# Optimization experiments

Measured on AMD Instinct MI355X. Metric: run time of the kernel, lower is better.

The kernel has to match this reference:

```python
import jax, jax.numpy as jnp
import numpy as np
from jax import lax

KS = 3
N = KS * KS


def _conv(x, W, b, pad, stride):
    out = lax.conv_general_dilated(
        x, W, window_strides=(stride, stride),
        padding=[(pad, pad), (pad, pad)],
        dimension_numbers=("NCHW", "OIHW", "NCHW"))
    return out + b[None, :, None, None]


def setup_inputs() -> dict:
    key = jax.random.key(0)
    ks = jax.random.split(key, 5)
    b, c, h, w, outc = 16, 64, 64, 64, 128
    return {
        "x": jax.random.normal(ks[0], (b, c, h, w), jnp.float32),
        "W_off": jax.random.normal(ks[1], (2 * N, c, KS, KS), jnp.float32) * 0.05,
        "b_off": jax.random.normal(ks[2], (2 * N,), jnp.float32) * 0.05,
        "W_k": jax.random.normal(ks[3], (outc, c, KS, KS), jnp.float32) * 0.05,
        "b_k": jax.random.normal(ks[4], (outc,), jnp.float32) * 0.05,
    }


def _deform_conv(x, W_off, b_off, W_k, b_k):
    b, c, h, w = x.shape
    offset = _conv(x, W_off, b_off, pad=1, stride=1)  # [b, 2N, h, w]

    # kernel-grid offsets, flattened with x (row) index first: n = i*ks + j
    rng = jnp.arange(KS, dtype=x.dtype) - (KS - 1) // 2  # [-1, 0, 1]
    pnx = jnp.repeat(rng, KS)  # [N]
    pny = jnp.tile(rng, KS)    # [N]

    # sampling positions p = p0 + p_n + offset, clamped into the image
    px = jnp.arange(h, dtype=x.dtype)[None, None, :, None] + pnx[None, :, None, None] + offset[:, :N]
    py = jnp.arange(w, dtype=x.dtype)[None, None, None, :] + pny[None, :, None, None] + offset[:, N:]
    px = jnp.clip(px, 0, h - 1)
    py = jnp.clip(py, 0, w - 1)

    fx = jnp.floor(px)
    fy = jnp.floor(py)
    tx = px - fx  # fractional parts (bilinear weights)
    ty = py - fy
    x0 = fx.astype(jnp.int32)
    y0 = fy.astype(jnp.int32)
    x1 = jnp.minimum(x0 + 1, h - 1)  # out-of-range tap carries zero weight
    y1 = jnp.minimum(y0 + 1, w - 1)

    x_hw = x.transpose(0, 2, 3, 1).reshape(b, h * w, c)  # [b, hw, c]

    def gather(ix, iy):
        idx = (ix * w + iy).reshape(b, -1, 1)  # [b, N*h*w, 1]
        return jnp.take_along_axis(x_hw, idx, axis=1).reshape(b, N, h, w, c)

    wx0, wx1 = (1 - tx)[..., None], tx[..., None]
    wy0, wy1 = (1 - ty)[..., None], ty[..., None]
    # 4-tap bilinear interpolation == the original's sparse G @ x
    xo = (gather(x0, y0) * wx0 * wy0 + gather(x1, y0) * wx1 * wy0
          + gather(x0, y1) * wx0 * wy1 + gather(x1, y1) * wx1 * wy1)  # [b,N,h,w,c]

    # _reshape_x_offset: out[b,c, i_h*ks+i, i_w*ks+j] = xo[b, i*ks+j, i_h, i_w, c]
    xo = xo.reshape(b, KS, KS, h, w, c).transpose(0, 5, 3, 1, 4, 2)
    xo = xo.reshape(b, c, h * KS, w * KS)

    return _conv(xo, W_k, b_k, pad=0, stride=KS)  # [b, outc, h, w]


def reference(x, W_off, b_off, W_k, b_k):
    return _deform_conv(x, W_off, b_off, W_k, b_k)
```

## Files before the change

### kernel.cpp

```cpp
#include <hip/hip_runtime.h>

typedef __attribute__((ext_vector_type(8))) short bf16x8;
typedef __attribute__((ext_vector_type(4))) float floatx4;

__device__ __forceinline__ unsigned short f2bf(float f) {
    unsigned int u = __float_as_uint(f);
    u += 0x7FFFu + ((u >> 16) & 1u);
    return (unsigned short)(u >> 16);
}

__device__ __forceinline__ int interp_word(int a00, int a01, int a10, int a11,
                                           float w00, float w01, float w10, float w11) {
    float vl = w00 * __uint_as_float((unsigned)a00 << 16)
             + w01 * __uint_as_float((unsigned)a01 << 16)
             + w10 * __uint_as_float((unsigned)a10 << 16)
             + w11 * __uint_as_float((unsigned)a11 << 16);
    float vh = w00 * __uint_as_float((unsigned)a00 & 0xffff0000u)
             + w01 * __uint_as_float((unsigned)a01 & 0xffff0000u)
             + w10 * __uint_as_float((unsigned)a10 & 0xffff0000u)
             + w11 * __uint_as_float((unsigned)a11 & 0xffff0000u);
    return (int)__builtin_amdgcn_perm(__float_as_uint(vh) + 0x8000u,
                                      __float_as_uint(vl) + 0x8000u, 0x07060302u);
}

__global__ __launch_bounds__(256) void prep_all(const float* __restrict__ x,
        const float* __restrict__ Wk, const float* __restrict__ Woff,
        unsigned short* __restrict__ xt, unsigned short* __restrict__ Wkb2,
        unsigned short* __restrict__ Woffb) {
    int bb = blockIdx.x;
    if (bb < 1024) {
        __shared__ float tile[64][65];
        int b = bb >> 6, y = bb & 63;
        const float* src = x + (size_t)b * 262144 + y * 64;
        int tx = threadIdx.x & 15, tg = threadIdx.x >> 4;
#pragma unroll
        for (int i = 0; i < 4; i++) {
            int c = tg + i * 16;
            float4 v = *(const float4*)(src + (size_t)c * 4096 + tx * 4);
            tile[c][tx * 4 + 0] = v.x; tile[c][tx * 4 + 1] = v.y;
            tile[c][tx * 4 + 2] = v.z; tile[c][tx * 4 + 3] = v.w;
        }
        __syncthreads();
        unsigned short* dst = xt + (size_t)bb * 4096;
#pragma unroll
        for (int i = 0; i < 4; i++) {
            int xc = tg + i * 16;
            int c4 = tx * 4;
            ushort4 v;
            v.x = f2bf(tile[c4 + 0][xc]); v.y = f2bf(tile[c4 + 1][xc]);
            v.z = f2bf(tile[c4 + 2][xc]); v.w = f2bf(tile[c4 + 3][xc]);
            *(ushort4*)(dst + xc * 64 + c4) = v;
        }
    } else if (bb < 1312) {
        int idx = (bb - 1024) * 256 + threadIdx.x;
        int tap = idx >> 13;
        int r = idx & 8191;
        int tile = r >> 9;
        int ln = (r >> 3) & 63;
        int j = r & 7;
        int mt = tile >> 1, kc = tile & 1;
        int oc = mt * 16 + (ln & 15);
        int c = kc * 32 + (ln >> 4) * 8 + j;
        Wkb2[idx] = f2bf(Wk[(oc * 64 + c) * 9 + tap]);
    } else {
        int idx = (bb - 1312) * 256 + threadIdx.x;
        int tap = idx >> 11;
        int r = idx & 2047;
        int tile = r >> 9;
        int ln = (r >> 3) & 63;
        int j = r & 7;
        int mt = tile >> 1, kc = tile & 1;
        int n = mt * 16 + (ln & 15);
        int c = kc * 32 + (ln >> 4) * 8 + j;
        float v = (n < 18) ? Woff[(n * 64 + c) * 9 + tap] : 0.f;
        Woffb[idx] = f2bf(v);
    }
}

__global__ __launch_bounds__(256, 2) void fused_kernel(
        const unsigned short* __restrict__ xt,
        const unsigned short* __restrict__ Wkb2,
        const unsigned short* __restrict__ Woffb,
        const float* __restrict__ boff,
        const float* __restrict__ bias,
        float* __restrict__ out) {
    __shared__ float offs[64][20];
    int tid = threadIdx.x;
    int wave = tid >> 6, lane = tid & 63;
    int frow = lane & 15, quad = lane >> 4;
    int bb = blockIdx.x;
    int xcd = bb & 7, idx = bb >> 3;
    int b = xcd * 2 + (idx >> 6);
    int pxBase = (idx & 63) * 64;
    int pl = wave * 16 + frow;
    int px = pxBase + pl;
    int y = px >> 6, xx = px & 63;
    const char* img = (const char*)(xt + (size_t)b * 262144) + quad * 16;

    float bv[2][4];
#pragma unroll
    for (int mt = 0; mt < 2; mt++)
#pragma unroll
        for (int rg = 0; rg < 4; rg++) {
            int n = mt * 16 + quad * 4 + rg;
            bv[mt][rg] = (n < 18) ? boff[n] : 0.f;
        }

    floatx4 acc1[2];
    acc1[0] = (floatx4)(0.f); acc1[1] = (floatx4)(0.f);
#pragma unroll
    for (int tap = 0; tap < 9; tap++) {
        int ry = y + tap / 3 - 1, rx = xx + tap % 3 - 1;
        bool valid = (ry >= 0) & (ry < 64) & (rx >= 0) & (rx < 64);
        const char* src = img + ((ry * 64 + rx) << 7);
        const unsigned short* wofft = Woffb + tap * 2048 + lane * 8;
        bf16x8 bz = {};
#pragma unroll
        for (int kc = 0; kc < 2; kc++) {
            bf16x8 bfr = valid ? *(const bf16x8*)(src + kc * 64) : bz;
#pragma unroll
            for (int mt = 0; mt < 2; mt++) {
                bf16x8 af = *(const bf16x8*)(wofft + (mt * 2 + kc) * 512);
                acc1[mt] = __builtin_amdgcn_mfma_f32_16x16x32_bf16(af, bfr, acc1[mt], 0, 0, 0);
            }
        }
    }
#pragma unroll
    for (int mt = 0; mt < 2; mt++)
#pragma unroll
        for (int rg = 0; rg < 4; rg++) {
            int n = mt * 16 + quad * 4 + rg;
            if (n < 18) offs[pl][n] = acc1[mt][rg] + bv[mt][rg];
        }
    __syncthreads();

    floatx4 acc[8];
#pragma unroll
    for (int i = 0; i < 8; i++) acc[i] = (floatx4)(0.f);

    const float* op = &offs[pl][0];

    auto stage = [&](int tap, int4 (&r00)[2], int4 (&r01)[2], int4 (&r10)[2],
                     int4 (&r11)[2], floatx4& w) {
        float orow = op[tap];
        float ocol = op[9 + tap];
        float pr = (float)(y + tap / 3 - 1) + orow;
        float pc = (float)(xx + tap % 3 - 1) + ocol;
        pr = fminf(fmaxf(pr, 0.f), 63.f);
        pc = fminf(fmaxf(pc, 0.f), 63.f);
        float fr = floorf(pr), fc = floorf(pc);
        float tr = pr - fr, tc = pc - fc;
        int r0 = (int)fr, c0 = (int)fc;
        int r1 = min(r0 + 1, 63), c1 = min(c0 + 1, 63);
        w[0] = (1.f - tr) * (1.f - tc);
        w[1] = (1.f - tr) * tc;
        w[2] = tr * (1.f - tc);
        w[3] = tr * tc;
        const char* p00 = img + ((r0 * 64 + c0) << 7);
        const char* p01 = img + ((r0 * 64 + c1) << 7);
        const char* p10 = img + ((r1 * 64 + c0) << 7);
        const char* p11 = img + ((r1 * 64 + c1) << 7);
#pragma unroll
        for (int kc = 0; kc < 2; kc++) {
            r00[kc] = *(const int4*)(p00 + kc * 64);
            r01[kc] = *(const int4*)(p01 + kc * 64);
            r10[kc] = *(const int4*)(p10 + kc * 64);
            r11[kc] = *(const int4*)(p11 + kc * 64);
        }
    };

    int4 c00[2], c01[2], c10[2], c11[2];
    floatx4 cw;
    stage(0, c00, c01, c10, c11, cw);

#pragma unroll 1
    for (int tap = 0; tap < 9; tap++) {
        const unsigned short* wkt = Wkb2 + tap * 8192 + lane * 8;

        bf16x8 af0[8];
#pragma unroll
        for (int mt = 0; mt < 8; mt++)
            af0[mt] = *(const bf16x8*)(wkt + (mt * 2) * 512);

        int4 n00[2], n01[2], n10[2], n11[2];
        floatx4 nw;
        if (tap < 8)
            stage(tap + 1, n00, n01, n10, n11, nw);

        bf16x8 bfrag[2];
#pragma unroll
        for (int kc = 0; kc < 2; kc++) {
            int4 r;
            r.x = interp_word(c00[kc].x, c01[kc].x, c10[kc].x, c11[kc].x,
                              cw[0], cw[1], cw[2], cw[3]);
            r.y = interp_word(c00[kc].y, c01[kc].y, c10[kc].y, c11[kc].y,
                              cw[0], cw[1], cw[2], cw[3]);
            r.z = interp_word(c00[kc].z, c01[kc].z, c10[kc].z, c11[kc].z,
                              cw[0], cw[1], cw[2], cw[3]);
            r.w = interp_word(c00[kc].w, c01[kc].w, c10[kc].w, c11[kc].w,
                              cw[0], cw[1], cw[2], cw[3]);
            bfrag[kc] = __builtin_bit_cast(bf16x8, r);
        }

#pragma unroll
        for (int mt = 0; mt < 8; mt++)
            acc[mt] = __builtin_amdgcn_mfma_f32_16x16x32_bf16(af0[mt], bfrag[0], acc[mt], 0, 0, 0);

        bf16x8 af1[8];
#pragma unroll
        for (int mt = 0; mt < 8; mt++)
            af1[mt] = *(const bf16x8*)(wkt + (mt * 2 + 1) * 512);
#pragma unroll
        for (int mt = 0; mt < 8; mt++)
            acc[mt] = __builtin_amdgcn_mfma_f32_16x16x32_bf16(af1[mt], bfrag[1], acc[mt], 0, 0, 0);

        if (tap < 8) {
#pragma unroll
            for (int kc = 0; kc < 2; kc++) {
                c00[kc] = n00[kc]; c01[kc] = n01[kc];
                c10[kc] = n10[kc]; c11[kc] = n11[kc];
            }
            cw = nw;
        }
    }

    float* outb = out + (size_t)b * 524288 + px;
#pragma unroll
    for (int mt = 0; mt < 8; mt++) {
        float4 bc = *(const float4*)(bias + mt * 16 + quad * 4);
        float bcv[4] = {bc.x, bc.y, bc.z, bc.w};
#pragma unroll
        for (int rg = 0; rg < 4; rg++) {
            int oc = mt * 16 + quad * 4 + rg;
            outb[oc * 4096] = acc[mt][rg] + bcv[rg];
        }
    }
}

extern "C" void kernel_launch(void* const* d_in, const int* in_sizes, int n_in,
                              void* d_out, int out_size, void* d_ws, size_t ws_size,
                              hipStream_t stream) {
    const float* x    = (const float*)d_in[0];
    const float* Woff = (const float*)d_in[1];
    const float* boff = (const float*)d_in[2];
    const float* Wk   = (const float*)d_in[3];
    const float* bk   = (const float*)d_in[4];
    float* out = (float*)d_out;

    char* ws = (char*)d_ws;
    unsigned short* xt    = (unsigned short*)ws;
    unsigned short* Wkb2  = (unsigned short*)(ws + 8388608);
    unsigned short* Woffb = (unsigned short*)(ws + 8536064);

    prep_all<<<1384, 256, 0, stream>>>(x, Wk, Woff, xt, Wkb2, Woffb);
    fused_kernel<<<1024, 256, 0, stream>>>(xt, Wkb2, Woffb, boff, bk, out);
}
```

Measured before the change: 144.5 us.

## Double-buffer tap weights in LDS via async global-to-LDS loads

Per-tap Wk fragments are now staged into two LDS buffers with global_load_lds and read back from LDS for the MFMAs, replacing the per-lane global loads. The weight loads for the next tap overlap with the gather and interpolation for the current tap. Synchronisation uses a manual s_waitcnt vmcnt plus s_barrier, and occupancy is raised to 3 blocks per CU. Risks are about 32KB of extra LDS per block limiting occupancy, the hand-counted vmcnt being fragile, and the removed __syncthreads before offs is read relying on the first barrier inside the loop.

```diff
diff --git a/kernel.cpp b/kernel.cpp
--- a/kernel.cpp
+++ b/kernel.cpp
@@ -21,6 +21,12 @@
              + w11 * __uint_as_float((unsigned)a11 & 0xffff0000u);
     return (int)__builtin_amdgcn_perm(__float_as_uint(vh) + 0x8000u,
                                       __float_as_uint(vl) + 0x8000u, 0x07060302u);
+}
+
+__device__ __forceinline__ void g2l16(const unsigned short* g, unsigned short* l) {
+    __builtin_amdgcn_global_load_lds(
+        (const __attribute__((address_space(1))) unsigned int*)g,
+        (__attribute__((address_space(3))) unsigned int*)l, 16, 0, 0);
 }
 
 __global__ __launch_bounds__(256) void prep_all(const float* __restrict__ x,
@@ -77,13 +83,15 @@
     }
 }
 
-__global__ __launch_bounds__(256, 2) void fused_kernel(
+__global__ __launch_bounds__(256, 3) void fused_kernel(
         const unsigned short* __restrict__ xt,
         const unsigned short* __restrict__ Wkb2,
         const unsigned short* __restrict__ Woffb,
         const float* __restrict__ boff,
         const float* __restrict__ bias,
         float* __restrict__ out) {
+    __shared__ unsigned short As0[8192];
+    __shared__ unsigned short As1[8192];
     __shared__ float offs[64][20];
     int tid = threadIdx.x;
     int wave = tid >> 6, lane = tid & 63;
@@ -132,7 +140,6 @@
             int n = mt * 16 + quad * 4 + rg;
             if (n < 18) offs[pl][n] = acc1[mt][rg] + bv[mt][rg];
         }
-    __syncthreads();
 
     floatx4 acc[8];
 #pragma unroll
@@ -169,60 +176,75 @@
         }
     };
 
-    int4 c00[2], c01[2], c10[2], c11[2];
-    floatx4 cw;
-    stage(0, c00, c01, c10, c11, cw);
-
-#pragma unroll 1
-    for (int tap = 0; tap < 9; tap++) {
-        const unsigned short* wkt = Wkb2 + tap * 8192 + lane * 8;
-
-        bf16x8 af0[8];
-#pragma unroll
-        for (int mt = 0; mt < 8; mt++)
-            af0[mt] = *(const bf16x8*)(wkt + (mt * 2) * 512);
-
-        int4 n00[2], n01[2], n10[2], n11[2];
-        floatx4 nw;
-        if (tap < 8)
-            stage(tap + 1, n00, n01, n10, n11, nw);
-
-        bf16x8 bfrag[2];
+    auto makeB = [&](int4 (&a00)[2], int4 (&a01)[2], int4 (&a10)[2], int4 (&a11)[2],
+                     floatx4& w, bf16x8& b0, bf16x8& b1) {
 #pragma unroll
         for (int kc = 0; kc < 2; kc++) {
             int4 r;
-            r.x = interp_word(c00[kc].x, c01[kc].x, c10[kc].x, c11[kc].x,
-                              cw[0], cw[1], cw[2], cw[3]);
-            r.y = interp_word(c00[kc].y, c01[kc].y, c10[kc].y, c11[kc].y,
-                              cw[0], cw[1], cw[2], cw[3]);
-            r.z = interp_word(c00[kc].z, c01[kc].z, c10[kc].z, c11[kc].z,
-                              cw[0], cw[1], cw[2], cw[3]);
-            r.w = interp_word(c00[kc].w, c01[kc].w, c10[kc].w, c11[kc].w,
-                              cw[0], cw[1], cw[2], cw[3]);
-            bfrag[kc] = __builtin_bit_cast(bf16x8, r);
-        }
-
-#pragma unroll
-        for (int mt = 0; mt < 8; mt++)
-            acc[mt] = __builtin_amdgcn_mfma_f32_16x16x32_bf16(af0[mt], bfrag[0], acc[mt], 0, 0, 0);
-
-        bf16x8 af1[8];
-#pragma unroll
-        for (int mt = 0; mt < 8; mt++)
-            af1[mt] = *(const bf16x8*)(wkt + (mt * 2 + 1) * 512);
-#pragma unroll
-        for (int mt = 0; mt < 8; mt++)
-            acc[mt] = __builtin_amdgcn_mfma_f32_16x16x32_bf16(af1[mt], bfrag[1], acc[mt], 0, 0, 0);
-
-        if (tap < 8) {
-#pragma unroll
-            for (int kc = 0; kc < 2; kc++) {
-                c00[kc] = n00[kc]; c01[kc] = n01[kc];
-                c10[kc] = n10[kc]; c11[kc] = n11[kc];
-            }
-            cw = nw;
-        }
-    }
+            r.x = interp_word(a00[kc].x, a01[kc].x, a10[kc].x, a11[kc].x, w[0], w[1], w[2], w[3]);
+            r.y = interp_word(a00[kc].y, a01[kc].y, a10[kc].y, a11[kc].y, w[0], w[1], w[2], w[3]);
+            r.z = interp_word(a00[kc].z, a01[kc].z, a10[kc].z, a11[kc].z, w[0], w[1], w[2], w[3]);
+            r.w = interp_word(a00[kc].w, a01[kc].w, a10[kc].w, a11[kc].w, w[0], w[1], w[2], w[3]);
+            if (kc == 0) b0 = __builtin_bit_cast(bf16x8, r);
+            else         b1 = __builtin_bit_cast(bf16x8, r);
+        }
+    };
+
+    int4 c00[2], c01[2], c10[2], c11[2];
+    int4 n00[2], n01[2], n10[2], n11[2];
+    floatx4 cw, nw;
+
+#define STAGE_A(BUF, TAP) do {                                                 \
+        const unsigned short* gs_ = Wkb2 + (TAP) * 8192 + wave * 2048 + lane * 8; \
+        g2l16(gs_,         &BUF[wave * 2048]);                                 \
+        g2l16(gs_ + 512,   &BUF[wave * 2048 + 512]);                           \
+        g2l16(gs_ + 1024,  &BUF[wave * 2048 + 1024]);                          \
+        g2l16(gs_ + 1536,  &BUF[wave * 2048 + 1536]);                          \
+    } while (0)
+
+#define BODY(TAP, RBUF, WBUF, LAST) do {                                       \
+        asm volatile("s_waitcnt vmcnt(8)\n\ts_barrier" ::: "memory");          \
+        if (!(LAST)) { STAGE_A(WBUF, (TAP) + 1); }                             \
+        __builtin_amdgcn_sched_barrier(0);                                     \
+        if (!(LAST)) stage((TAP) + 1, n00, n01, n10, n11, nw);                 \
+        __builtin_amdgcn_sched_barrier(0);                                     \
+        bf16x8 bf0, bf1;                                                       \
+        makeB(c00, c01, c10, c11, cw, bf0, bf1);                               \
+        _Pragma("unroll")                                                      \
+        for (int mt = 0; mt < 8; mt++) {                                       \
+            bf16x8 af = *(const bf16x8*)&RBUF[(mt * 2) * 512 + lane * 8];      \
+            acc[mt] = __builtin_amdgcn_mfma_f32_16x16x32_bf16(af, bf0, acc[mt], 0, 0, 0); \
+        }                                                                      \
+        _Pragma("unroll")                                                      \
+        for (int mt = 0; mt < 8; mt++) {                                       \
+            bf16x8 af = *(const bf16x8*)&RBUF[(mt * 2 + 1) * 512 + lane * 8];  \
+            acc[mt] = __builtin_amdgcn_mfma_f32_16x16x32_bf16(af, bf1, acc[mt], 0, 0, 0); \
+        }                                                                      \
+        if (!(LAST)) {                                                         \
+            _Pragma("unroll")                                                  \
+            for (int kc = 0; kc < 2; kc++) {                                   \
+                c00[kc] = n00[kc]; c01[kc] = n01[kc];                          \
+                c10[kc] = n10[kc]; c11[kc] = n11[kc];                          \
+            }                                                                  \
+            cw = nw;                                                           \
+        }                                                                      \
+    } while (0)
+
+    __builtin_amdgcn_sched_barrier(0);
+    STAGE_A(As0, 0);
+    __builtin_amdgcn_sched_barrier(0);
+    stage(0, c00, c01, c10, c11, cw);
+
+#pragma unroll 1
+    for (int t2 = 0; t2 < 4; t2++) {
+        int tap = t2 * 2;
+        BODY(tap,     As0, As1, false);
+        BODY(tap + 1, As1, As0, false);
+    }
+    BODY(8, As0, As1, true);
+
+#undef BODY
+#undef STAGE_A
 
     float* outb = out + (size_t)b * 524288 + px;
 #pragma unroll
```

Result: faster. 134.2 us (-7.1%).
